# Kernel tuning notes

Hardware: AMD Instinct MI355X
Metric: run time of the kernel (lower is better)

The kernel has to match this reference:

```python
import jax, jax.numpy as jnp
import numpy as np

DX = 1.0      # grid spacing
RHO = 1.0     # density
NU = 0.1      # viscosity
DT = 0.1      # timestep
STEPS = 1000  # Jacobi relaxation iterations

# Periodic (CIRCULAR) finite-difference stencils via jnp.roll on the last two axes.

def ddx(f):
    # central difference along x (axis -2)
    return (jnp.roll(f, -1, axis=-2) - jnp.roll(f, 1, axis=-2)) / (2.0 * DX)

def ddy(f):
    # central difference along y (axis -1)
    return (jnp.roll(f, -1, axis=-1) - jnp.roll(f, 1, axis=-1)) / (2.0 * DX)

def neighbor_sum(f):
    # 4-neighbor sum: LapInv stencil used by the Jacobi step
    return (jnp.roll(f, 1, axis=-2) + jnp.roll(f, -1, axis=-2)
            + jnp.roll(f, 1, axis=-1) + jnp.roll(f, -1, axis=-1))

def laplacian(f):
    # 5-point Laplacian / dx^2
    return (neighbor_sum(f) - 4.0 * f) / (DX * DX)


def setup_inputs() -> dict:
    key = jax.random.key(0)
    k1, k2 = jax.random.split(key)
    X = jax.random.normal(k1, (2, 1, 512, 512), dtype=jnp.float32)
    forcing = jax.random.normal(k2, (2, 1, 512, 512), dtype=jnp.float32)
    t = jnp.zeros((), dtype=jnp.float32)
    return {"t": t, "X": X, "forcing": forcing}


def reference(t, X, forcing):
    # advection (v . grad) v : X[0]*dXi/dx + X[1]*dXi/dy, broadcast over vector dim
    adv = X[0] * ddx(X) + X[1] * ddy(X)              # (2, C, H, W)
    partial = -adv + NU * laplacian(X) + forcing      # (2, C, H, W)
    # divergence of partial -> pressure Poisson RHS
    B = RHO * (ddx(partial[0]) + ddy(partial[1])) / DT  # (C, H, W)

    def poisson_jacobi_step(phi, _):
        phi = (neighbor_sum(phi) - B * (DX * DX)) / 4.0
        return phi, None

    phi, _ = jax.lax.scan(poisson_jacobi_step, B, xs=None, length=STEPS)
    grad_phi = jnp.stack([ddx(phi), ddy(phi)])        # (2, C, H, W)
    return partial - grad_phi / RHO
```

## Files before the change

### kernel.cpp

```cpp
#include <hip/hip_runtime.h>
#include <math.h>


#define HH 512
#define WW 512
#define NCELL (HH * WW)
#define NU_C 0.1f
#define INV_DT 10.0f
#define PI_F 3.14159265358979323846f

__device__ __forceinline__ void cell_idx(int idx, int& i, int& j,
                                         int& ip, int& im, int& jp, int& jm) {
    i = idx >> 9;
    j = idx & 511;
    ip = (i + 1) & 511;
    im = (i + 511) & 511;
    jp = (j + 1) & 511;
    jm = (j + 511) & 511;
}

__global__ __launch_bounds__(256) void partial_kernel(const float* __restrict__ X,
                                                      const float* __restrict__ F,
                                                      float* __restrict__ p) {
    int idx = blockIdx.x * blockDim.x + threadIdx.x;
    int i, j, ip, im, jp, jm;
    cell_idx(idx, i, j, ip, im, jp, jm);

    float x0c = X[idx];
    float x1c = X[NCELL + idx];

#pragma unroll
    for (int c = 0; c < 2; ++c) {
        const float* Xc = X + c * NCELL;
        float xc  = Xc[idx];
        float xip = Xc[ip * WW + j];
        float xim = Xc[im * WW + j];
        float xjp = Xc[i * WW + jp];
        float xjm = Xc[i * WW + jm];
        float ddx = (xip - xim) * 0.5f;
        float ddy = (xjp - xjm) * 0.5f;
        float lap = xip + xim + xjp + xjm - 4.0f * xc;
        float adv = x0c * ddx + x1c * ddy;
        p[c * NCELL + idx] = -adv + NU_C * lap + F[c * NCELL + idx];
    }
}

__device__ float2* fft512_lds(float2* a, float2* b, const float2* tw, int t) {
    float2* src = a;
    float2* dst = b;
#pragma unroll
    for (int s = 0; s < 9; ++s) {
        int Ls = 1 << s;
        int pp = t & (Ls - 1);
        int q  = t >> s;
        float2 w = tw[pp << (8 - s)];
        float2 xa = src[q * Ls + pp];
        float2 xb = src[q * Ls + pp + 256];
        float2 wb;
        wb.x = w.x * xb.x - w.y * xb.y;
        wb.y = w.x * xb.y + w.y * xb.x;
        dst[q * 2 * Ls + pp]      = make_float2(xa.x + wb.x, xa.y + wb.y);
        dst[q * 2 * Ls + pp + Ls] = make_float2(xa.x - wb.x, xa.y - wb.y);
        float2* tmp = src; src = dst; dst = tmp;
        __syncthreads();
    }
    return src;
}

__device__ __forceinline__ void build_tw(float2* tw, int t, float sign) {
    float ang = sign * (-PI_F) * (float)t * (1.0f / 256.0f);
    float sn, cs;
    sincosf(ang, &sn, &cs);
    tw[t] = make_float2(cs, sn);
}

__global__ __launch_bounds__(256) void fwd_rows(const float* __restrict__ p,
                                                float2* __restrict__ Z) {
    __shared__ float2 bufA[512], bufB[512], tw[256];
    int i = blockIdx.x, t = threadIdx.x;
    build_tw(tw, t, 1.0f);
    bufA[t]       = make_float2(p[i * WW + t],       p[NCELL + i * WW + t]);
    bufA[t + 256] = make_float2(p[i * WW + t + 256], p[NCELL + i * WW + t + 256]);
    __syncthreads();
    float2* res = fft512_lds(bufA, bufB, tw, t);
    Z[i * WW + t]       = res[t];
    Z[i * WW + t + 256] = res[t + 256];
}

__global__ __launch_bounds__(256) void fwd_cols(const float2* __restrict__ Z,
                                                float2* __restrict__ Z2) {
    __shared__ float2 bufA[512], bufB[512], tw[256];
    int j = blockIdx.x, t = threadIdx.x;
    build_tw(tw, t, 1.0f);
    bufA[t]       = Z[t * WW + j];
    bufA[t + 256] = Z[(t + 256) * WW + j];
    __syncthreads();
    float2* res = fft512_lds(bufA, bufB, tw, t);
    Z2[t * WW + j]       = res[t];
    Z2[(t + 256) * WW + j] = res[t + 256];
}

__global__ __launch_bounds__(256) void pw_inv_cols(const float2* __restrict__ Z2,
                                                   float2* __restrict__ W1) {
    __shared__ float2 bufA[512], bufB[512], tw[256];
    int j = blockIdx.x, t = threadIdx.x;
    int mj = (WW - j) & 511;
    build_tw(tw, t, -1.0f);

    double aj = 2.0 * M_PI * (double)j / 512.0;
    double cj = cos(aj);
    float  syf = (float)sin(aj);

#pragma unroll
    for (int e = 0; e < 2; ++e) {
        int ki = t + e * 256;
        int mi = (HH - ki) & 511;
        float2 z  = Z2[ki * WW + j];
        float2 zm = Z2[mi * WW + mj];

        double ai = 2.0 * M_PI * (double)ki / 512.0;
        double s4 = 2.0 * cos(ai) + 2.0 * cj;
        double beta = 0.0;
        if (!(ki == 0 && j == 0)) {
            double r  = 0.25 * s4;
            double rN = pow(fabs(r), 1000.0);
            double M  = rN - (1.0 - rN) / (4.0 - s4);
            beta = -10.0 * M / (512.0 * 512.0);
        }
        float sx = (float)sin(ai);
        float su  = sx * sx + syf * syf;
        float u2x = sx * sx - syf * syf;
        float u2y = 2.0f * sx * syf;
        float cx = zm.x, cy = -zm.y;
        float tx = u2x * cx - u2y * cy;
        float ty = u2x * cy + u2y * cx;
        float bh = (float)(0.5 * beta);
        bufA[ki] = make_float2(bh * (su * z.x + tx), bh * (su * z.y + ty));
    }
    __syncthreads();
    float2* res = fft512_lds(bufA, bufB, tw, t);
    W1[t * WW + j]         = res[t];
    W1[(t + 256) * WW + j] = res[t + 256];
}

__global__ __launch_bounds__(256) void inv_rows_out(const float2* __restrict__ W1,
                                                    const float* __restrict__ p,
                                                    float* __restrict__ out) {
    __shared__ float2 bufA[512], bufB[512], tw[256];
    int i = blockIdx.x, t = threadIdx.x;
    build_tw(tw, t, -1.0f);
    bufA[t]       = W1[i * WW + t];
    bufA[t + 256] = W1[i * WW + t + 256];
    __syncthreads();
    float2* res = fft512_lds(bufA, bufB, tw, t);
#pragma unroll
    for (int e = 0; e < 2; ++e) {
        int j = t + e * 256;
        float2 w = res[j];
        out[i * WW + j]         = p[i * WW + j]         - w.x;
        out[NCELL + i * WW + j] = p[NCELL + i * WW + j] - w.y;
    }
}

extern "C" void kernel_launch(void* const* d_in, const int* in_sizes, int n_in,
                              void* d_out, int out_size, void* d_ws, size_t ws_size,
                              hipStream_t stream) {
    const float* X = (const float*)d_in[1];
    const float* F = (const float*)d_in[2];
    float* out = (float*)d_out;
    float* ws  = (float*)d_ws;

    float*  p    = ws;
    float2* bufZ = (float2*)(ws + 2 * NCELL);
    float2* bufZ2 = bufZ + NCELL;

    dim3 blk(256);
    partial_kernel<<<dim3(NCELL / 256), blk, 0, stream>>>(X, F, p);
    fwd_rows     <<<dim3(HH), blk, 0, stream>>>(p, bufZ);
    fwd_cols     <<<dim3(WW), blk, 0, stream>>>(bufZ, bufZ2);
    pw_inv_cols  <<<dim3(WW), blk, 0, stream>>>(bufZ2, bufZ);
    inv_rows_out <<<dim3(HH), blk, 0, stream>>>(bufZ, p, out);
}
```

Baseline: 89.82 us.

## Fuse FFT Poisson pipeline into one cooperative kernel with grid syncs

Merges the stencil, forward FFTs, spectral multiply and inverse FFTs into a single cooperative kernel of 512 blocks with grid-wide syncs. There is a three-kernel fallback if the cooperative launch fails. The partial stencil is folded into the row-FFT phase, and row FFT results are written transposed so the column pass reads contiguously. The column phase recomputes the mirrored column's FFT locally instead of reading a strided global buffer. Double-precision cos/pow in the spectral multiplier is replaced by float sincos plus exp/log1p, which reduces FP64 work but may lose accuracy near the spectral singularities, and grid.sync plus 2-block occupancy add synchronisation risk.

Result: slower. 209.0 us (+132.7%).

```diff
diff --git a/kernel.cpp b/kernel.cpp
--- a/kernel.cpp
+++ b/kernel.cpp
@@ -1,51 +1,25 @@
 #include <hip/hip_runtime.h>
+#include <hip/hip_cooperative_groups.h>
 #include <math.h>
+
+namespace cg = cooperative_groups;
 
 
 #define HH 512
 #define WW 512
 #define NCELL (HH * WW)
 #define NU_C 0.1f
-#define INV_DT 10.0f
 #define PI_F 3.14159265358979323846f
 
-__device__ __forceinline__ void cell_idx(int idx, int& i, int& j,
-                                         int& ip, int& im, int& jp, int& jm) {
-    i = idx >> 9;
-    j = idx & 511;
-    ip = (i + 1) & 511;
-    im = (i + 511) & 511;
-    jp = (j + 1) & 511;
-    jm = (j + 511) & 511;
-}
-
-__global__ __launch_bounds__(256) void partial_kernel(const float* __restrict__ X,
-                                                      const float* __restrict__ F,
-                                                      float* __restrict__ p) {
-    int idx = blockIdx.x * blockDim.x + threadIdx.x;
-    int i, j, ip, im, jp, jm;
-    cell_idx(idx, i, j, ip, im, jp, jm);
-
-    float x0c = X[idx];
-    float x1c = X[NCELL + idx];
-
-#pragma unroll
-    for (int c = 0; c < 2; ++c) {
-        const float* Xc = X + c * NCELL;
-        float xc  = Xc[idx];
-        float xip = Xc[ip * WW + j];
-        float xim = Xc[im * WW + j];
-        float xjp = Xc[i * WW + jp];
-        float xjm = Xc[i * WW + jm];
-        float ddx = (xip - xim) * 0.5f;
-        float ddy = (xjp - xjm) * 0.5f;
-        float lap = xip + xim + xjp + xjm - 4.0f * xc;
-        float adv = x0c * ddx + x1c * ddy;
-        p[c * NCELL + idx] = -adv + NU_C * lap + F[c * NCELL + idx];
-    }
-}
-
-__device__ float2* fft512_lds(float2* a, float2* b, const float2* tw, int t) {
+struct Smem {
+    float2 bufA[512];
+    float2 bufB[512];
+    float2 zm[512];
+    float2 tw[256];
+};
+
+__device__ __forceinline__ float2* fft512(float2* a, float2* b,
+                                          const float2* tw, int t, float sgn) {
     float2* src = a;
     float2* dst = b;
 #pragma unroll
@@ -54,105 +28,123 @@
         int pp = t & (Ls - 1);
         int q  = t >> s;
         float2 w = tw[pp << (8 - s)];
+        float wy = sgn * w.y;
         float2 xa = src[q * Ls + pp];
         float2 xb = src[q * Ls + pp + 256];
-        float2 wb;
-        wb.x = w.x * xb.x - w.y * xb.y;
-        wb.y = w.x * xb.y + w.y * xb.x;
-        dst[q * 2 * Ls + pp]      = make_float2(xa.x + wb.x, xa.y + wb.y);
-        dst[q * 2 * Ls + pp + Ls] = make_float2(xa.x - wb.x, xa.y - wb.y);
+        float wbx = w.x * xb.x - wy * xb.y;
+        float wby = w.x * xb.y + wy * xb.x;
+        dst[q * 2 * Ls + pp]      = make_float2(xa.x + wbx, xa.y + wby);
+        dst[q * 2 * Ls + pp + Ls] = make_float2(xa.x - wbx, xa.y - wby);
         float2* tmp = src; src = dst; dst = tmp;
         __syncthreads();
     }
     return src;
 }
 
-__device__ __forceinline__ void build_tw(float2* tw, int t, float sign) {
-    float ang = sign * (-PI_F) * (float)t * (1.0f / 256.0f);
+__device__ __forceinline__ void build_tw(Smem& sm, int t) {
+    float ang = -PI_F * (float)t * (1.0f / 256.0f);
     float sn, cs;
     sincosf(ang, &sn, &cs);
-    tw[t] = make_float2(cs, sn);
-}
-
-__global__ __launch_bounds__(256) void fwd_rows(const float* __restrict__ p,
-                                                float2* __restrict__ Z) {
-    __shared__ float2 bufA[512], bufB[512], tw[256];
-    int i = blockIdx.x, t = threadIdx.x;
-    build_tw(tw, t, 1.0f);
-    bufA[t]       = make_float2(p[i * WW + t],       p[NCELL + i * WW + t]);
-    bufA[t + 256] = make_float2(p[i * WW + t + 256], p[NCELL + i * WW + t + 256]);
-    __syncthreads();
-    float2* res = fft512_lds(bufA, bufB, tw, t);
-    Z[i * WW + t]       = res[t];
-    Z[i * WW + t + 256] = res[t + 256];
-}
-
-__global__ __launch_bounds__(256) void fwd_cols(const float2* __restrict__ Z,
-                                                float2* __restrict__ Z2) {
-    __shared__ float2 bufA[512], bufB[512], tw[256];
-    int j = blockIdx.x, t = threadIdx.x;
-    build_tw(tw, t, 1.0f);
-    bufA[t]       = Z[t * WW + j];
-    bufA[t + 256] = Z[(t + 256) * WW + j];
-    __syncthreads();
-    float2* res = fft512_lds(bufA, bufB, tw, t);
-    Z2[t * WW + j]       = res[t];
-    Z2[(t + 256) * WW + j] = res[t + 256];
-}
-
-__global__ __launch_bounds__(256) void pw_inv_cols(const float2* __restrict__ Z2,
-                                                   float2* __restrict__ W1) {
-    __shared__ float2 bufA[512], bufB[512], tw[256];
-    int j = blockIdx.x, t = threadIdx.x;
+    sm.tw[t] = make_float2(cs, sn);
+}
+
+__device__ void phaseA(Smem& sm, int i, int t,
+                       const float* __restrict__ X, const float* __restrict__ F,
+                       float* __restrict__ p, float2* __restrict__ Zt) {
+    build_tw(sm, t);
+    int ip = (i + 1) & 511, im = (i + 511) & 511;
+    const float* X0 = X;
+    const float* X1 = X + NCELL;
+#pragma unroll
+    for (int e = 0; e < 2; ++e) {
+        int j = t + e * 256;
+        int jp = (j + 1) & 511, jm = (j + 511) & 511;
+        float x0c = X0[i * WW + j], x1c = X1[i * WW + j];
+        float aip = X0[ip * WW + j], aim = X0[im * WW + j];
+        float ajp = X0[i * WW + jp], ajm = X0[i * WW + jm];
+        float p0 = -(x0c * (aip - aim) * 0.5f + x1c * (ajp - ajm) * 0.5f)
+                 + NU_C * (aip + aim + ajp + ajm - 4.0f * x0c) + F[i * WW + j];
+        float bip = X1[ip * WW + j], bim = X1[im * WW + j];
+        float bjp = X1[i * WW + jp], bjm = X1[i * WW + jm];
+        float p1 = -(x0c * (bip - bim) * 0.5f + x1c * (bjp - bjm) * 0.5f)
+                 + NU_C * (bip + bim + bjp + bjm - 4.0f * x1c) + F[NCELL + i * WW + j];
+        p[i * WW + j] = p0;
+        p[NCELL + i * WW + j] = p1;
+        sm.bufA[j] = make_float2(p0, p1);
+    }
+    __syncthreads();
+    float2* res = fft512(sm.bufA, sm.bufB, sm.tw, t, 1.0f);
+    Zt[t * 512 + i]         = res[t];
+    Zt[(t + 256) * 512 + i] = res[t + 256];
+}
+
+__device__ void phaseB(Smem& sm, int j, int t,
+                       const float2* __restrict__ Zt, float2* __restrict__ W1) {
+    build_tw(sm, t);
     int mj = (WW - j) & 511;
-    build_tw(tw, t, -1.0f);
-
-    double aj = 2.0 * M_PI * (double)j / 512.0;
-    double cj = cos(aj);
-    float  syf = (float)sin(aj);
-
+    sm.bufA[t]       = Zt[mj * 512 + t];
+    sm.bufA[t + 256] = Zt[mj * 512 + t + 256];
+    __syncthreads();
+    float2* res = fft512(sm.bufA, sm.bufB, sm.tw, t, 1.0f);
+    sm.zm[t]       = res[t];
+    sm.zm[t + 256] = res[t + 256];
+    __syncthreads();
+    sm.bufA[t]       = Zt[j * 512 + t];
+    sm.bufA[t + 256] = Zt[j * 512 + t + 256];
+    __syncthreads();
+    res = fft512(sm.bufA, sm.bufB, sm.tw, t, 1.0f);
+
+    float shy, chy;
+    sincosf(PI_F * (float)j * (1.0f / 512.0f), &shy, &chy);
+    float sy = 2.0f * shy * chy;
+    float qy = shy * shy;
+    float Wx[2], Wy[2];
 #pragma unroll
     for (int e = 0; e < 2; ++e) {
         int ki = t + e * 256;
         int mi = (HH - ki) & 511;
-        float2 z  = Z2[ki * WW + j];
-        float2 zm = Z2[mi * WW + mj];
-
-        double ai = 2.0 * M_PI * (double)ki / 512.0;
-        double s4 = 2.0 * cos(ai) + 2.0 * cj;
-        double beta = 0.0;
-        if (!(ki == 0 && j == 0)) {
-            double r  = 0.25 * s4;
-            double rN = pow(fabs(r), 1000.0);
-            double M  = rN - (1.0 - rN) / (4.0 - s4);
-            beta = -10.0 * M / (512.0 * 512.0);
+        float shx, chx;
+        sincosf(PI_F * (float)ki * (1.0f / 512.0f), &shx, &chx);
+        float sx = 2.0f * shx * chx;
+        float qx = shx * shx;
+        float qs = qx + qy;
+        float beta = 0.0f;
+        if (ki != 0 || j != 0) {
+            float rN;
+            if (qs < 1.0f)      rN = expf(1000.0f * log1pf(-qs));
+            else if (qs > 1.0f) rN = expf(1000.0f * logf(qs - 1.0f));
+            else                rN = 0.0f;
+            float M = rN - (1.0f - rN) / (4.0f * qs);
+            beta = -10.0f * M * (1.0f / (512.0f * 512.0f));
         }
-        float sx = (float)sin(ai);
-        float su  = sx * sx + syf * syf;
-        float u2x = sx * sx - syf * syf;
-        float u2y = 2.0f * sx * syf;
-        float cx = zm.x, cy = -zm.y;
+        float su  = sx * sx + sy * sy;
+        float u2x = sx * sx - sy * sy;
+        float u2y = 2.0f * sx * sy;
+        float2 z  = res[ki];
+        float2 zc = sm.zm[mi];
+        float cx = zc.x, cy = -zc.y;
         float tx = u2x * cx - u2y * cy;
         float ty = u2x * cy + u2y * cx;
-        float bh = (float)(0.5 * beta);
-        bufA[ki] = make_float2(bh * (su * z.x + tx), bh * (su * z.y + ty));
-    }
-    __syncthreads();
-    float2* res = fft512_lds(bufA, bufB, tw, t);
-    W1[t * WW + j]         = res[t];
-    W1[(t + 256) * WW + j] = res[t + 256];
-}
-
-__global__ __launch_bounds__(256) void inv_rows_out(const float2* __restrict__ W1,
-                                                    const float* __restrict__ p,
-                                                    float* __restrict__ out) {
-    __shared__ float2 bufA[512], bufB[512], tw[256];
-    int i = blockIdx.x, t = threadIdx.x;
-    build_tw(tw, t, -1.0f);
-    bufA[t]       = W1[i * WW + t];
-    bufA[t + 256] = W1[i * WW + t + 256];
-    __syncthreads();
-    float2* res = fft512_lds(bufA, bufB, tw, t);
+        float bh = 0.5f * beta;
+        Wx[e] = bh * (su * z.x + tx);
+        Wy[e] = bh * (su * z.y + ty);
+    }
+    sm.bufA[t]       = make_float2(Wx[0], Wy[0]);
+    sm.bufA[t + 256] = make_float2(Wx[1], Wy[1]);
+    __syncthreads();
+    res = fft512(sm.bufA, sm.bufB, sm.tw, t, -1.0f);
+    W1[t * 512 + j]         = res[t];
+    W1[(t + 256) * 512 + j] = res[t + 256];
+}
+
+__device__ void phaseC(Smem& sm, int i, int t,
+                       const float2* __restrict__ W1, const float* __restrict__ p,
+                       float* __restrict__ out) {
+    build_tw(sm, t);
+    sm.bufA[t]       = W1[i * 512 + t];
+    sm.bufA[t + 256] = W1[i * 512 + t + 256];
+    __syncthreads();
+    float2* res = fft512(sm.bufA, sm.bufB, sm.tw, t, -1.0f);
 #pragma unroll
     for (int e = 0; e < 2; ++e) {
         int j = t + e * 256;
@@ -160,6 +152,42 @@
         out[i * WW + j]         = p[i * WW + j]         - w.x;
         out[NCELL + i * WW + j] = p[NCELL + i * WW + j] - w.y;
     }
+}
+
+__global__ __launch_bounds__(256, 2) void fused_all(const float* __restrict__ X,
+                                                    const float* __restrict__ F,
+                                                    float* __restrict__ out,
+                                                    float* __restrict__ ws) {
+    __shared__ Smem sm;
+    cg::grid_group grid = cg::this_grid();
+    int b = blockIdx.x, t = threadIdx.x;
+    float*  p  = ws;
+    float2* Zt = (float2*)(ws + 2 * NCELL);
+    float2* W1 = Zt + NCELL;
+    phaseA(sm, b, t, X, F, p, Zt);
+    grid.sync();
+    phaseB(sm, b, t, Zt, W1);
+    grid.sync();
+    phaseC(sm, b, t, W1, p, out);
+}
+
+__global__ __launch_bounds__(256, 2) void kA(const float* __restrict__ X,
+                                             const float* __restrict__ F,
+                                             float* __restrict__ p,
+                                             float2* __restrict__ Zt) {
+    __shared__ Smem sm;
+    phaseA(sm, blockIdx.x, threadIdx.x, X, F, p, Zt);
+}
+__global__ __launch_bounds__(256, 2) void kB(const float2* __restrict__ Zt,
+                                             float2* __restrict__ W1) {
+    __shared__ Smem sm;
+    phaseB(sm, blockIdx.x, threadIdx.x, Zt, W1);
+}
+__global__ __launch_bounds__(256, 2) void kC(const float2* __restrict__ W1,
+                                             const float* __restrict__ p,
+                                             float* __restrict__ out) {
+    __shared__ Smem sm;
+    phaseC(sm, blockIdx.x, threadIdx.x, W1, p, out);
 }
 
 extern "C" void kernel_launch(void* const* d_in, const int* in_sizes, int n_in,
@@ -170,14 +198,17 @@
     float* out = (float*)d_out;
     float* ws  = (float*)d_ws;
 
-    float*  p    = ws;
-    float2* bufZ = (float2*)(ws + 2 * NCELL);
-    float2* bufZ2 = bufZ + NCELL;
-
-    dim3 blk(256);
-    partial_kernel<<<dim3(NCELL / 256), blk, 0, stream>>>(X, F, p);
-    fwd_rows     <<<dim3(HH), blk, 0, stream>>>(p, bufZ);
-    fwd_cols     <<<dim3(WW), blk, 0, stream>>>(bufZ, bufZ2);
-    pw_inv_cols  <<<dim3(WW), blk, 0, stream>>>(bufZ2, bufZ);
-    inv_rows_out <<<dim3(HH), blk, 0, stream>>>(bufZ, p, out);
-}
+    void* args[] = { (void*)&X, (void*)&F, (void*)&out, (void*)&ws };
+    hipError_t err = hipLaunchCooperativeKernel((const void*)fused_all,
+                                                dim3(512), dim3(256),
+                                                args, 0, stream);
+    if (err != hipSuccess) {
+        (void)hipGetLastError();
+        float*  p  = ws;
+        float2* Zt = (float2*)(ws + 2 * NCELL);
+        float2* W1 = Zt + NCELL;
+        kA<<<dim3(512), dim3(256), 0, stream>>>(X, F, p, Zt);
+        kB<<<dim3(512), dim3(256), 0, stream>>>(Zt, W1);
+        kC<<<dim3(512), dim3(256), 0, stream>>>(W1, p, out);
+    }
+}
```
